# Performance work log

Measured on AMD Instinct MI355X. Metric: run time of the kernel, lower is better.

## Reference

```python
import jax, jax.numpy as jnp
import numpy as np

N, D, S, M = 32, 128, 128, 64
BASIS = 5


def setup_inputs() -> dict:
    key = jax.random.key(0)
    k1, k2 = jax.random.split(key)
    inputs = jax.random.normal(k1, (N, D, M, M), dtype=jnp.float32)
    coeffs = jax.random.normal(k2, (D, S, BASIS), dtype=jnp.float32) * np.sqrt(2.0) / (D + S)
    all_bias = jnp.zeros((1, S, 1, 1), dtype=jnp.float32)
    return {"inputs": inputs, "coeffs": coeffs, "all_bias": all_bias}


def reference(inputs, coeffs, all_bias):
    # inputs: [N, D, m, m]
    m = inputs.shape[3]
    diag_part = jnp.diagonal(inputs, axis1=2, axis2=3)          # [N, D, m]
    mean_diag = jnp.mean(diag_part, axis=2, keepdims=True)      # [N, D, 1]
    mean_cols = jnp.mean(inputs, axis=2)                        # [N, D, m]
    mean_all = jnp.mean(mean_cols, axis=2)                      # [N, D]

    op1 = (mean_cols[:, :, :, None] + mean_cols[:, :, None, :]) / 2   # [N, D, m, m]
    op2 = inputs
    op3 = (diag_part[:, :, :, None] + diag_part[:, :, None, :]) / 2
    op4 = jnp.broadcast_to(mean_diag[:, :, :, None], inputs.shape)
    op5 = jnp.broadcast_to(mean_all[:, :, None, None], inputs.shape)

    ops_out = jnp.stack([op1, op2, op3, op4, op5], axis=2)      # [N, D, 5, m, m]
    output = jnp.einsum('dsb,ndbij->nsij', coeffs, ops_out)     # [N, S, m, m]
    return output + all_bias
```

## Files before the change

### kernel.cpp

```cpp
#include <hip/hip_runtime.h>

#define NN 32
#define DD 128
#define SS 128
#define MM 64
#define PP 4096
#define DSZ (DD * SS)

typedef short bf16x8 __attribute__((ext_vector_type(8)));
typedef float f32x4  __attribute__((ext_vector_type(4)));

#define OFF_CPK 0
#define OFF_C1T (OFF_CPK + 5 * DSZ)
#define OFF_MC  (OFF_C1T + DSZ / 2)
#define OFF_DG  (OFF_MC + NN * DD * MM)
#define OFF_MD  (OFF_DG + NN * DD * MM)
#define OFF_MA  (OFF_MD + NN * DD)
#define OFF_UP  (OFF_MA + NN * DD)

__device__ __forceinline__ unsigned int fbits(float f) {
    union { float f; unsigned int u; } c; c.f = f; return c.u;
}

__global__ __launch_bounds__(256) void pack_k(const float* __restrict__ coeffs,
                                              float* __restrict__ cpk,
                                              unsigned short* __restrict__ c1t) {
    int g = blockIdx.x * 256 + threadIdx.x;
    int d = g >> 7, s = g & 127;
    float v0 = coeffs[g * 5 + 0];
    float v1 = coeffs[g * 5 + 1];
    float v2 = coeffs[g * 5 + 2];
    float v3 = coeffs[g * 5 + 3];
    float v4 = coeffs[g * 5 + 4];
    cpk[0 * DSZ + g] = v0;
    cpk[2 * DSZ + g] = v2;
    cpk[3 * DSZ + g] = v3;
    cpk[4 * DSZ + g] = v4;
    unsigned int u = fbits(v1);
    u += 0x7fffu + ((u >> 16) & 1);
    c1t[s * DD + d] = (unsigned short)(u >> 16);
}

__global__ __launch_bounds__(256) void stats_k(const float* __restrict__ x,
                                               float* __restrict__ mc,
                                               float* __restrict__ dg,
                                               float* __restrict__ md,
                                               float* __restrict__ ma) {
    int nd = blockIdx.x * 4 + (threadIdx.x >> 6);
    int l  = threadIdx.x & 63;
    const float* base = x + (size_t)nd * PP;
    int iq = l >> 4, jq = l & 15;

    float4 cs = make_float4(0.f, 0.f, 0.f, 0.f);
    float dv = 0.f;
#pragma unroll
    for (int r = 0; r < 16; ++r) {
        float4 v = *(const float4*)(base + (r * 4 + iq) * MM + jq * 4);
        cs.x += v.x; cs.y += v.y; cs.z += v.z; cs.w += v.w;
        if (r == jq)
            dv = (iq == 0) ? v.x : (iq == 1) ? v.y : (iq == 2) ? v.z : v.w;
    }
#pragma unroll
    for (int m = 16; m <= 32; m <<= 1) {
        cs.x += __shfl_xor(cs.x, m);
        cs.y += __shfl_xor(cs.y, m);
        cs.z += __shfl_xor(cs.z, m);
        cs.w += __shfl_xor(cs.w, m);
    }
    if (iq == 0) {
        float4 o = make_float4(cs.x * (1.f / 64.f), cs.y * (1.f / 64.f),
                               cs.z * (1.f / 64.f), cs.w * (1.f / 64.f));
        *(float4*)(mc + nd * MM + jq * 4) = o;
    }
    dg[nd * MM + 4 * jq + iq] = dv;
    float dsum = dv;
#pragma unroll
    for (int m = 1; m <= 32; m <<= 1) dsum += __shfl_xor(dsum, m);
    float tot = cs.x + cs.y + cs.z + cs.w;
#pragma unroll
    for (int m = 1; m <= 8; m <<= 1) tot += __shfl_xor(tot, m);
    if (l == 0) {
        md[nd] = dsum * (1.f / 64.f);
        ma[nd] = tot * (1.f / 4096.f);
    }
}

__global__ __launch_bounds__(256) void combine_k(const float* __restrict__ cpk,
                                                 const float* __restrict__ mc,
                                                 const float* __restrict__ dg,
                                                 const float* __restrict__ md,
                                                 const float* __restrict__ ma,
                                                 const float* __restrict__ bias,
                                                 float* __restrict__ up) {
    int sg = blockIdx.x, n = blockIdx.y;
    int t  = threadIdx.x;
    int i  = t & 63;
    int sq = t >> 6;
    int s0 = sg * 16 + sq * 4;

    const float* c0p = cpk + 0 * DSZ;
    const float* c2p = cpk + 2 * DSZ;
    const float* c3p = cpk + 3 * DSZ;
    const float* c4p = cpk + 4 * DSZ;

    float wacc[4] = {0.f, 0.f, 0.f, 0.f};
    float vacc[4] = {0.f, 0.f, 0.f, 0.f};
#pragma unroll 2
    for (int d = 0; d < DD; ++d) {
        int bidx = (n * DD + d) * MM + i;
        float m  = mc[bidx];
        float g  = dg[bidx];
        float mdv = md[n * DD + d];
        float mav = ma[n * DD + d];
#pragma unroll
        for (int r = 0; r < 4; ++r) {
            int cs = d * SS + s0 + r;
            wacc[r] += c0p[cs] * m + c2p[cs] * g;
            vacc[r] += c3p[cs] * mdv + c4p[cs] * mav;
        }
    }
#pragma unroll
    for (int r = 0; r < 4; ++r) {
        int s = s0 + r;
        up[((size_t)n * SS + s) * MM + i] = 0.5f * (wacc[r] + vacc[r] + bias[s]);
    }
}

#define USTR 68
__global__ __launch_bounds__(256, 3) void gemm_k(const float* __restrict__ x,
                                                 const unsigned short* __restrict__ c1t,
                                                 const float* __restrict__ up,
                                                 float* __restrict__ out) {
    __shared__ float us[SS * USTR];

    int n  = blockIdx.y;
    int p0 = blockIdx.x * 128;
    int t  = threadIdx.x;
    int w  = t >> 6, l = t & 63;
    int wp = w & 1, wsn = w >> 1;
    int q  = l >> 4, c = l & 15;

    const float* upn = up + (size_t)n * SS * MM;
#pragma unroll
    for (int e = t; e < SS * MM / 4; e += 256) {
        int s  = e >> 4;
        int i4 = (e & 15) * 4;
        *(f32x4*)&us[s * USTR + i4] = *(const f32x4*)(upn + s * MM + i4);
    }
    __syncthreads();

    int p0w = p0 + wp * 64;
    int s0w = wsn * 64;
    int iw  = p0w >> 6;
    const float* xb = x + (size_t)n * DD * PP;

    f32x4 acc[4][4];
#pragma unroll
    for (int a = 0; a < 4; ++a)
#pragma unroll
        for (int b = 0; b < 4; ++b) acc[a][b] = (f32x4)0.f;

#pragma unroll
    for (int kt = 0; kt < 4; ++kt) {
        int k0 = kt * 32 + q * 8;
        bf16x8 af[4];
#pragma unroll
        for (int st = 0; st < 4; ++st)
            af[st] = *(const bf16x8*)(c1t + (size_t)(s0w + st * 16 + c) * DD + k0);
#pragma unroll
        for (int pt = 0; pt < 4; ++pt) {
            const float* xp = xb + (size_t)k0 * PP + (p0w + pt * 16 + c);
            float f0 = xp[0 * PP], f1 = xp[1 * PP], f2 = xp[2 * PP], f3 = xp[3 * PP];
            float f4 = xp[4 * PP], f5 = xp[5 * PP], f6 = xp[6 * PP], f7 = xp[7 * PP];
            union { unsigned int u[4]; bf16x8 v; } bb;
            bb.u[0] = __builtin_amdgcn_perm(fbits(f1), fbits(f0), 0x07060302u);
            bb.u[1] = __builtin_amdgcn_perm(fbits(f3), fbits(f2), 0x07060302u);
            bb.u[2] = __builtin_amdgcn_perm(fbits(f5), fbits(f4), 0x07060302u);
            bb.u[3] = __builtin_amdgcn_perm(fbits(f7), fbits(f6), 0x07060302u);
#pragma unroll
            for (int st = 0; st < 4; ++st)
                acc[st][pt] = __builtin_amdgcn_mfma_f32_16x16x32_bf16(af[st], bb.v,
                                                                     acc[st][pt], 0, 0, 0);
        }
    }

#pragma unroll
    for (int st = 0; st < 4; ++st) {
#pragma unroll
        for (int r = 0; r < 4; ++r) {
            int s = s0w + st * 16 + q * 4 + r;
            float uiv = us[s * USTR + iw];
            float* orow = out + ((size_t)(n * SS + s)) * PP;
#pragma unroll
            for (int pt = 0; pt < 4; ++pt) {
                int p = p0w + pt * 16 + c;
                int j = p & 63;
                orow[p] = acc[st][pt][r] + uiv + us[s * USTR + j];
            }
        }
    }
}

extern "C" void kernel_launch(void* const* d_in, const int* in_sizes, int n_in,
                              void* d_out, int out_size, void* d_ws, size_t ws_size,
                              hipStream_t stream) {
    const float* x      = (const float*)d_in[0];
    const float* coeffs = (const float*)d_in[1];
    const float* bias   = (const float*)d_in[2];
    float* out = (float*)d_out;
    float* ws  = (float*)d_ws;

    float*          cpk = ws + OFF_CPK;
    unsigned short* c1t = (unsigned short*)(ws + OFF_C1T);
    float*          mc  = ws + OFF_MC;
    float*          dg  = ws + OFF_DG;
    float*          md  = ws + OFF_MD;
    float*          ma  = ws + OFF_MA;
    float*          up  = ws + OFF_UP;

    pack_k<<<DSZ / 256, 256, 0, stream>>>(coeffs, cpk, c1t);
    stats_k<<<NN * DD / 4, 256, 0, stream>>>(x, mc, dg, md, ma);
    combine_k<<<dim3(8, NN), 256, 0, stream>>>(cpk, mc, dg, md, ma, bias, up);
    gemm_k<<<dim3(PP / 128, NN), 256, 0, stream>>>(x, c1t, up, out);
}
```

Measured before the change: 171.8 us.

## Stage bf16-converted x tile in swizzled LDS and merge pack with stats kernel

Measured after the change: 166.5 us. -3.1%, faster.

```diff
diff --git a/kernel.cpp b/kernel.cpp
--- a/kernel.cpp
+++ b/kernel.cpp
@@ -9,6 +9,7 @@
 
 typedef short bf16x8 __attribute__((ext_vector_type(8)));
 typedef float f32x4  __attribute__((ext_vector_type(4)));
+typedef unsigned int u32x2 __attribute__((ext_vector_type(2)));
 
 #define OFF_CPK 0
 #define OFF_C1T (OFF_CPK + 5 * DSZ)
@@ -22,30 +23,31 @@
     union { float f; unsigned int u; } c; c.f = f; return c.u;
 }
 
-__global__ __launch_bounds__(256) void pack_k(const float* __restrict__ coeffs,
-                                              float* __restrict__ cpk,
-                                              unsigned short* __restrict__ c1t) {
-    int g = blockIdx.x * 256 + threadIdx.x;
-    int d = g >> 7, s = g & 127;
-    float v0 = coeffs[g * 5 + 0];
-    float v1 = coeffs[g * 5 + 1];
-    float v2 = coeffs[g * 5 + 2];
-    float v3 = coeffs[g * 5 + 3];
-    float v4 = coeffs[g * 5 + 4];
-    cpk[0 * DSZ + g] = v0;
-    cpk[2 * DSZ + g] = v2;
-    cpk[3 * DSZ + g] = v3;
-    cpk[4 * DSZ + g] = v4;
-    unsigned int u = fbits(v1);
-    u += 0x7fffu + ((u >> 16) & 1);
-    c1t[s * DD + d] = (unsigned short)(u >> 16);
-}
-
-__global__ __launch_bounds__(256) void stats_k(const float* __restrict__ x,
-                                               float* __restrict__ mc,
-                                               float* __restrict__ dg,
-                                               float* __restrict__ md,
-                                               float* __restrict__ ma) {
+__global__ __launch_bounds__(256) void stats_pack_k(const float* __restrict__ x,
+                                                    const float* __restrict__ coeffs,
+                                                    float* __restrict__ cpk,
+                                                    unsigned short* __restrict__ c1t,
+                                                    float* __restrict__ mc,
+                                                    float* __restrict__ dg,
+                                                    float* __restrict__ md,
+                                                    float* __restrict__ ma) {
+    if (blockIdx.x >= (NN * DD / 4)) {
+        int g = (blockIdx.x - NN * DD / 4) * 256 + threadIdx.x;
+        int d = g >> 7, s = g & 127;
+        float v0 = coeffs[g * 5 + 0];
+        float v1 = coeffs[g * 5 + 1];
+        float v2 = coeffs[g * 5 + 2];
+        float v3 = coeffs[g * 5 + 3];
+        float v4 = coeffs[g * 5 + 4];
+        cpk[0 * DSZ + g] = v0;
+        cpk[2 * DSZ + g] = v2;
+        cpk[3 * DSZ + g] = v3;
+        cpk[4 * DSZ + g] = v4;
+        unsigned int u = fbits(v1);
+        u += 0x7fffu + ((u >> 16) & 1);
+        c1t[s * DD + d] = (unsigned short)(u >> 16);
+        return;
+    }
     int nd = blockIdx.x * 4 + (threadIdx.x >> 6);
     int l  = threadIdx.x & 63;
     const float* base = x + (size_t)nd * PP;
@@ -126,33 +128,51 @@
     }
 }
 
-#define USTR 68
 __global__ __launch_bounds__(256, 3) void gemm_k(const float* __restrict__ x,
                                                  const unsigned short* __restrict__ c1t,
                                                  const float* __restrict__ up,
                                                  float* __restrict__ out) {
-    __shared__ float us[SS * USTR];
+    __shared__ unsigned short xs[128 * 128];
 
     int n  = blockIdx.y;
     int p0 = blockIdx.x * 128;
     int t  = threadIdx.x;
-    int w  = t >> 6, l = t & 63;
+
+    {
+        int u  = t & 31;
+        int kq = t >> 5;
+        int pl = u * 4;
+        const float* xb = x + (size_t)n * DD * PP + p0 + pl;
+#pragma unroll
+        for (int pp = 0; pp < 4; ++pp) {
+            int k4 = pp * 32 + kq * 4;
+            float4 v0 = *(const float4*)(xb + (size_t)(k4 + 0) * PP);
+            float4 v1 = *(const float4*)(xb + (size_t)(k4 + 1) * PP);
+            float4 v2 = *(const float4*)(xb + (size_t)(k4 + 2) * PP);
+            float4 v3 = *(const float4*)(xb + (size_t)(k4 + 3) * PP);
+#pragma unroll
+            for (int i = 0; i < 4; ++i) {
+                float a0 = (i == 0) ? v0.x : (i == 1) ? v0.y : (i == 2) ? v0.z : v0.w;
+                float a1 = (i == 0) ? v1.x : (i == 1) ? v1.y : (i == 2) ? v1.z : v1.w;
+                float a2 = (i == 0) ? v2.x : (i == 1) ? v2.y : (i == 2) ? v2.z : v2.w;
+                float a3 = (i == 0) ? v3.x : (i == 1) ? v3.y : (i == 2) ? v3.z : v3.w;
+                int p = pl + i;
+                u32x2 wv;
+                wv.x = __builtin_amdgcn_perm(fbits(a1), fbits(a0), 0x07060302u);
+                wv.y = __builtin_amdgcn_perm(fbits(a3), fbits(a2), 0x07060302u);
+                int boff = (p * 256 + 2 * k4) ^ (((p ^ (p >> 3)) & 7) << 4);
+                *(u32x2*)((char*)xs + boff) = wv;
+            }
+        }
+    }
+    __syncthreads();
+
+    int w = t >> 6, l = t & 63;
     int wp = w & 1, wsn = w >> 1;
-    int q  = l >> 4, c = l & 15;
-
-    const float* upn = up + (size_t)n * SS * MM;
-#pragma unroll
-    for (int e = t; e < SS * MM / 4; e += 256) {
-        int s  = e >> 4;
-        int i4 = (e & 15) * 4;
-        *(f32x4*)&us[s * USTR + i4] = *(const f32x4*)(upn + s * MM + i4);
-    }
-    __syncthreads();
-
+    int q = l >> 4, c = l & 15;
+    int s0w = wsn * 64;
     int p0w = p0 + wp * 64;
-    int s0w = wsn * 64;
-    int iw  = p0w >> 6;
-    const float* xb = x + (size_t)n * DD * PP;
+    int plw = wp * 64;
 
     f32x4 acc[4][4];
 #pragma unroll
@@ -167,35 +187,37 @@
 #pragma unroll
         for (int st = 0; st < 4; ++st)
             af[st] = *(const bf16x8*)(c1t + (size_t)(s0w + st * 16 + c) * DD + k0);
+
+        bf16x8 bfr[4];
 #pragma unroll
         for (int pt = 0; pt < 4; ++pt) {
-            const float* xp = xb + (size_t)k0 * PP + (p0w + pt * 16 + c);
-            float f0 = xp[0 * PP], f1 = xp[1 * PP], f2 = xp[2 * PP], f3 = xp[3 * PP];
-            float f4 = xp[4 * PP], f5 = xp[5 * PP], f6 = xp[6 * PP], f7 = xp[7 * PP];
-            union { unsigned int u[4]; bf16x8 v; } bb;
-            bb.u[0] = __builtin_amdgcn_perm(fbits(f1), fbits(f0), 0x07060302u);
-            bb.u[1] = __builtin_amdgcn_perm(fbits(f3), fbits(f2), 0x07060302u);
-            bb.u[2] = __builtin_amdgcn_perm(fbits(f5), fbits(f4), 0x07060302u);
-            bb.u[3] = __builtin_amdgcn_perm(fbits(f7), fbits(f6), 0x07060302u);
+            int p = plw + pt * 16 + c;
+            int boff = (p * 256 + 2 * k0) ^ (((p ^ (p >> 3)) & 7) << 4);
+            bfr[pt] = *(const bf16x8*)((const char*)xs + boff);
+        }
+
+#pragma unroll
+        for (int pt = 0; pt < 4; ++pt)
 #pragma unroll
             for (int st = 0; st < 4; ++st)
-                acc[st][pt] = __builtin_amdgcn_mfma_f32_16x16x32_bf16(af[st], bb.v,
+                acc[st][pt] = __builtin_amdgcn_mfma_f32_16x16x32_bf16(af[st], bfr[pt],
                                                                      acc[st][pt], 0, 0, 0);
-        }
-    }
-
+    }
+
+    int iw = p0w >> 6;
+    const float* upn = up + (size_t)n * SS * MM;
 #pragma unroll
     for (int st = 0; st < 4; ++st) {
 #pragma unroll
         for (int r = 0; r < 4; ++r) {
             int s = s0w + st * 16 + q * 4 + r;
-            float uiv = us[s * USTR + iw];
-            float* orow = out + ((size_t)(n * SS + s)) * PP;
+            const float* urow = upn + (size_t)s * MM;
+            float uiv = urow[iw];
+            float* orow = out + ((size_t)(n * SS + s)) * PP + p0w;
 #pragma unroll
             for (int pt = 0; pt < 4; ++pt) {
-                int p = p0w + pt * 16 + c;
-                int j = p & 63;
-                orow[p] = acc[st][pt][r] + uiv + us[s * USTR + j];
+                int j = pt * 16 + c;
+                orow[j] = acc[st][pt][r] + uiv + urow[j];
             }
         }
     }
@@ -218,8 +240,8 @@
     float*          ma  = ws + OFF_MA;
     float*          up  = ws + OFF_UP;
 
-    pack_k<<<DSZ / 256, 256, 0, stream>>>(coeffs, cpk, c1t);
-    stats_k<<<NN * DD / 4, 256, 0, stream>>>(x, mc, dg, md, ma);
+    stats_pack_k<<<NN * DD / 4 + DSZ / 256, 256, 0, stream>>>(x, coeffs, cpk, c1t,
+                                                              mc, dg, md, ma);
     combine_k<<<dim3(8, NN), 256, 0, stream>>>(cpk, mc, dg, md, ma, bias, up);
     gemm_k<<<dim3(PP / 128, NN), 256, 0, stream>>>(x, c1t, up, out);
 }
```
